# Kernel optimization log

Hardware: AMD Instinct MI355X
Metric: run time of the kernel (lower is better)

The kernel has to match this reference:

```python
import jax, jax.numpy as jnp
import numpy as np

B = 8192
SIZES = [784, 1024, 512, 10]
LR = 0.001          # update_rate default in forward
CYCLES = 60         # hardcoded in PCN.forward


def _xavier(k, shape):
    # torch.nn.init.xavier_uniform_ for 2D: fan_in=shape[1], fan_out=shape[0]
    bound = np.sqrt(6.0 / (shape[0] + shape[1])).astype(np.float32)
    return jax.random.uniform(k, shape, jnp.float32, -bound, bound)


def setup_inputs() -> dict:
    key = jax.random.key(0)
    ks = jax.random.split(key, 7)
    input_data = jax.random.uniform(ks[0], (B, SIZES[0]), jnp.float32)
    s1 = _xavier(ks[1], (B, SIZES[1]))
    s2 = _xavier(ks[2], (B, SIZES[2]))
    s3 = _xavier(ks[3], (B, SIZES[3]))
    W1 = _xavier(ks[4], (SIZES[0], SIZES[1]))
    W2 = _xavier(ks[5], (SIZES[1], SIZES[2]))
    W3 = _xavier(ks[6], (SIZES[2], SIZES[3]))
    return dict(input_data=input_data, s1=s1, s2=s2, s3=s3, W1=W1, W2=W2, W3=W3)


def _sig_prime(x):
    s = jax.nn.sigmoid(x)
    return s * (1.0 - s)


def reference(input_data, s1, s2, s3, W1, W2, W3):
    def cycle(carry, _):
        s1, s2, s3, _ = carry
        # predictions: layer i predicts layer i-1 via sigmoid(state_i) @ W_i.T
        p0 = jax.nn.sigmoid(s1) @ W1.T            # (B, 784)
        p1 = jax.nn.sigmoid(s2) @ W2.T            # (B, 1024)
        p2 = jax.nn.sigmoid(s3) @ W3.T            # (B, 512)
        e0 = input_data - p0
        e1 = s1 - p1
        e2 = s2 - p2
        # state updates (batched matmul (W.T @ e) == e @ W)
        s1n = s1 + LR * (-e1 + _sig_prime(s1) * (e0 @ W1))
        s2n = s2 + LR * (-e2 + _sig_prime(s2) * (e1 @ W2))
        s3n = s3 + LR * (_sig_prime(s3) * (e2 @ W3))  # last layer: no -e term
        return (s1n, s2n, s3n, p0), None

    p0_init = jnp.zeros((B, SIZES[0]), jnp.float32)
    (s1, s2, s3, p0_last), _ = jax.lax.scan(
        cycle, (s1, s2, s3, p0_init), None, length=CYCLES)
    # returns (last-layer state, predictions[0] from the final cycle)
    return s3, p0_last
```

## Files before the change

### kernel.cpp

```cpp
#include <hip/hip_runtime.h>
#include <hip/hip_bf16.h>

typedef __bf16 bf16x8 __attribute__((ext_vector_type(8)));
typedef ushort ushort8 __attribute__((ext_vector_type(8)));
typedef float  f32x4  __attribute__((ext_vector_type(4)));

#define LR_C 0.001f
#define VMCNT(n) asm volatile("s_waitcnt vmcnt(" #n ")" ::: "memory")
#define CFENCE() asm volatile("" ::: "memory")

__device__ __forceinline__ float sigf(float x){ return 1.0f/(1.0f + __expf(-x)); }
__device__ __forceinline__ ushort f2bu(float x){ __hip_bfloat16 h = __float2bfloat16(x); return *(ushort*)&h; }
__device__ __forceinline__ float bu2f(ushort u){ __hip_bfloat16 h = *(__hip_bfloat16*)&u; return __bfloat162float(h); }

__device__ __forceinline__ void gload_lds16(const void* g, void* l){
  __builtin_amdgcn_global_load_lds(
      (const __attribute__((address_space(1))) void*)g,
      (__attribute__((address_space(3))) void*)l, 16, 0, 0);
}


__global__ void k_cvt_bf16(__hip_bfloat16* dst, const float* src, int n){
  int i = blockIdx.x*256 + threadIdx.x;
  if (i < n) dst[i] = __float2bfloat16(src[i]);
}

__global__ void k_cvt_pad(__hip_bfloat16* dst, const float* src, int rows, int cs, int cd){
  int i = blockIdx.x*256 + threadIdx.x;
  if (i >= rows*cd) return;
  int r = i / cd, c = i % cd;
  float v = (c < cs) ? src[r*cs + c] : 0.0f;
  dst[i] = __float2bfloat16(v);
}

__global__ void k_transpose(__hip_bfloat16* dst, const float* src, int sr, int sc, int dstride){
  int i = blockIdx.x*256 + threadIdx.x;
  if (i >= sc*dstride) return;
  int n = i / dstride, j = i % dstride;
  float v = (j < sr) ? src[j*sc + n] : 0.0f;
  dst[i] = __float2bfloat16(v);
}

__global__ void k_init_state(ushort* sf, __hip_bfloat16* A, const float* s, int n){
  int i = blockIdx.x*256 + threadIdx.x;
  if (i >= n) return;
  float v = s[i];
  sf[i] = f2bu(v);
  A[i] = __float2bfloat16(sigf(v));
}

__global__ void k_init_s3(float* s3f, __hip_bfloat16* A3, const float* s3){
  int i = blockIdx.x*256 + threadIdx.x;
  if (i >= 8192*32) return;
  int b = i >> 5, c = i & 31;
  if (c < 10){
    float v = s3[b*10 + c];
    s3f[b*10 + c] = v;
    A3[i] = __float2bfloat16(sigf(v));
  } else {
    A3[i] = __float2bfloat16(0.0f);
  }
}

__global__ void k_zero_bf16(__hip_bfloat16* p, int n){
  int i = blockIdx.x*256 + threadIdx.x;
  if (i < n) p[i] = __float2bfloat16(0.0f);
}

__global__ void k_copy_f32(float* dst, const float* src, int n){
  int i = blockIdx.x*256 + threadIdx.x;
  if (i < n) dst[i] = src[i];
}


__device__ __forceinline__ void gemm128(
    const ushort* __restrict__ A, const ushort* __restrict__ B,
    int lda, int ldb, int K, int Nclamp,
    int brow, int bcol, int t, ushort* As, ushort* Bs, f32x4 (&acc)[4][4])
{
  const int w    = t >> 6;
  const int lane = t & 63;
  const int wr   = (w >> 1) * 64;
  const int wc   = (w & 1) * 64;
  const int fr   = lane & 15;
  const int ks   = (lane >> 4) * 8;
  const int rks  = ks ^ ((fr & 3) << 3);

#pragma unroll
  for (int m=0;m<4;m++)
#pragma unroll
    for (int n=0;n<4;n++){ acc[m][n][0]=0.f; acc[m][n][1]=0.f; acc[m][n][2]=0.f; acc[m][n][3]=0.f; }

  const int arow = t >> 2;
  const int acol = ((t & 3) * 8) ^ ((arow & 3) << 3);
  const ushort* gA  = A + (size_t)(brow + arow) * lda + acol;
  const ushort* gA2 = gA + (size_t)64 * lda;
  int rb  = bcol + arow;      if (rb  > Nclamp-1) rb  = Nclamp-1;
  int rb2 = bcol + 64 + arow; if (rb2 > Nclamp-1) rb2 = Nclamp-1;
  const ushort* gB  = B + (size_t)rb  * ldb + acol;
  const ushort* gB2 = B + (size_t)rb2 * ldb + acol;

  auto STAGE = [&](int buf, int k0){
    ushort* Ab = As + buf*4096;
    ushort* Bb = Bs + buf*4096;
    gload_lds16(gA  + k0, Ab + w*512);
    gload_lds16(gA2 + k0, Ab + 2048 + w*512);
    gload_lds16(gB  + k0, Bb + w*512);
    gload_lds16(gB2 + k0, Bb + 2048 + w*512);
  };

  const int nt = K >> 5;
  STAGE(0, 0);
  if (nt > 1) STAGE(1, 32);
  if (nt > 2) STAGE(2, 64);

  int cur = 0;
  for (int tk = 0; tk < nt; ++tk){
    const int rem = nt - 1 - tk;
    if (rem >= 2)      { VMCNT(8); }
    else if (rem == 1) { VMCNT(4); }
    else               { VMCNT(0); }
    __builtin_amdgcn_s_barrier();
    CFENCE();

    const ushort* Ab = As + cur*4096;
    const ushort* Bb = Bs + cur*4096;
    bf16x8 af[4], bfv[4];
#pragma unroll
    for (int m=0;m<4;m++) af[m]  = *(const bf16x8*)&Ab[(wr + m*16 + fr)*32 + rks];
#pragma unroll
    for (int n=0;n<4;n++) bfv[n] = *(const bf16x8*)&Bb[(wc + n*16 + fr)*32 + rks];
#pragma unroll
    for (int m=0;m<4;m++)
#pragma unroll
      for (int n=0;n<4;n++)
        acc[m][n] = __builtin_amdgcn_mfma_f32_16x16x32_bf16(af[m], bfv[n], acc[m][n], 0, 0, 0);

    CFENCE();
    __builtin_amdgcn_s_barrier();
    CFENCE();
    if (tk + 3 < nt) STAGE(cur, (tk+3)*32);
    cur = cur + 1; if (cur == 3) cur = 0;
  }
}

__device__ __forceinline__ void stageC(const f32x4 (&acc)[4][4], int t, ushort* Cs){
  const int w = t >> 6, lane = t & 63;
  const int wr = (w >> 1) * 64, wc = (w & 1) * 64;
  const int fr = lane & 15, r4 = (lane >> 4) * 4;
#pragma unroll
  for (int m=0;m<4;m++){
#pragma unroll
    for (int j=0;j<4;j++){
      int r = wr + m*16 + r4 + j;
      int sw = (r & 3) << 3;
#pragma unroll
      for (int n=0;n<4;n++){
        int c = wc + n*16 + fr;
        Cs[r*128 + (c ^ sw)] = f2bu(acc[m][n][j]);
      }
    }
  }
}

__device__ __forceinline__ void blockmap(int lid, int nbx, int& brow, int& bcol){
  int by = (lid & 7) + 8 * ((lid >> 3) / nbx);
  int bx = (lid >> 3) % nbx;
  brow = by * 128; bcol = bx * 128;
}


__global__ __launch_bounds__(256, 3)
void fusedD1(int base,
             const ushort* __restrict__ A1, const ushort* __restrict__ W1b,
             const ushort* __restrict__ inb, ushort* __restrict__ e0, float* p0out,
             const ushort* __restrict__ e1b, const ushort* __restrict__ W2T,
             ushort* __restrict__ s2f, const ushort* __restrict__ e2b,
             ushort* __restrict__ A2,
             const ushort* __restrict__ W3T, float* __restrict__ s3f,
             ushort* __restrict__ A3)
{
  __shared__ __align__(16) ushort lds[3*4096*2];
  ushort* As = lds;
  ushort* Bs = lds + 3*4096;
  ushort* Cs = lds;
  const int bid = blockIdx.x + base;
  const int t = threadIdx.x;
  const int lr = t >> 4, lc = (t & 15) * 8;
  f32x4 acc[4][4];

  if (bid < 448){
    int brow, bcol; blockmap(bid, 7, brow, bcol);
    gemm128(A1, W1b, 1024, 1024, 1024, 784, brow, bcol, t, As, Bs, acc);
    stageC(acc, t, Cs); __syncthreads();
#pragma unroll
    for (int it=0; it<8; ++it){
      int r = it*16 + lr, gr = brow + r, gc = bcol + lc;
      if (gc < 784){
        ushort8 ib = *(const ushort8*)&inb[(size_t)gr*784 + gc];
        ushort8 g  = *(const ushort8*)&Cs[r*128 + (lc ^ ((r&3)<<3))];
        ushort8 e; float pv0,pv1,pv2,pv3,pv4,pv5,pv6,pv7;
        pv0=bu2f(g[0]); pv1=bu2f(g[1]); pv2=bu2f(g[2]); pv3=bu2f(g[3]);
        pv4=bu2f(g[4]); pv5=bu2f(g[5]); pv6=bu2f(g[6]); pv7=bu2f(g[7]);
        e[0]=f2bu(bu2f(ib[0])-pv0); e[1]=f2bu(bu2f(ib[1])-pv1);
        e[2]=f2bu(bu2f(ib[2])-pv2); e[3]=f2bu(bu2f(ib[3])-pv3);
        e[4]=f2bu(bu2f(ib[4])-pv4); e[5]=f2bu(bu2f(ib[5])-pv5);
        e[6]=f2bu(bu2f(ib[6])-pv6); e[7]=f2bu(bu2f(ib[7])-pv7);
        *(ushort8*)&e0[(size_t)gr*800 + gc] = e;
        if (p0out){
          f32x4 lo = {pv0,pv1,pv2,pv3}, hi = {pv4,pv5,pv6,pv7};
          *(f32x4*)&p0out[(size_t)gr*784 + gc]     = lo;
          *(f32x4*)&p0out[(size_t)gr*784 + gc + 4] = hi;
        }
      }
    }
  } else if (bid < 704){
    int brow, bcol; blockmap(bid - 448, 4, brow, bcol);
    gemm128(e1b, W2T, 1024, 1024, 1024, 512, brow, bcol, t, As, Bs, acc);
    stageC(acc, t, Cs); __syncthreads();
#pragma unroll
    for (int it=0; it<8; ++it){
      int r = it*16 + lr, gr = brow + r, gc = bcol + lc;
      size_t ix = (size_t)gr*512 + gc;
      ushort8 sv = *(const ushort8*)&s2f[ix];
      ushort8 e2 = *(const ushort8*)&e2b[ix];
      ushort8 g = *(const ushort8*)&Cs[r*128 + (lc ^ ((r&3)<<3))];
      ushort8 a2o, so;
#pragma unroll
      for (int k=0;k<8;k++){
        float s = bu2f(sv[k]); float a = sigf(s);
        float ap = a*(1.0f-a);
        float d = LR_C*(-bu2f(e2[k]) + ap*bu2f(g[k]));
        so[k] = f2bu(s + d);
        a2o[k] = f2bu(a + ap*d);
      }
      *(ushort8*)&s2f[ix] = so;
      *(ushort8*)&A2[ix] = a2o;
    }
  } else {
    int brow = (bid - 704) * 128;
    gemm128(e2b, W3T, 512, 512, 512, 16, brow, 0, t, As, Bs, acc);
    const int w = t >> 6, lane = t & 63;
    const int wr = (w >> 1) * 64, wc = (w & 1) * 64;
    const int fr = lane & 15, r4 = (lane >> 4) * 4;
    const int orow0 = brow + wr + r4, ocol0 = wc + fr;
#pragma unroll
    for (int m=0;m<4;m++)
#pragma unroll
      for (int n=0;n<4;n++){
        int col = ocol0 + n*16;
        if (col >= 10) continue;
#pragma unroll
        for (int j=0;j<4;j++){
          int row = orow0 + m*16 + j;
          float s = s3f[(size_t)row*10 + col];
          float a = sigf(s);
          float ap = a*(1.0f-a);
          float d = LR_C*(ap*acc[m][n][j]);
          s3f[(size_t)row*10 + col] = s + d;
          A3[(size_t)row*32 + col] = f2bu(a + ap*d);
        }
      }
  }
}

__global__ __launch_bounds__(256, 3)
void fusedD2(const ushort* __restrict__ A2, const ushort* __restrict__ W2b,
             const ushort* __restrict__ e0, const ushort* __restrict__ W1T,
             ushort* __restrict__ s1f, ushort* __restrict__ A1,
             ushort* __restrict__ e1b,
             const ushort* __restrict__ A3, const ushort* __restrict__ W3b,
             const ushort* __restrict__ s2f, ushort* __restrict__ e2b)
{
  __shared__ __align__(16) ushort lds[3*4096*2];
  ushort* As = lds;
  ushort* Bs = lds + 3*4096;
  ushort* Cs = lds;
  const int bid = blockIdx.x;
  const int t = threadIdx.x;
  const int lr = t >> 4, lc = (t & 15) * 8;
  f32x4 acc[4][4];

  if (bid < 512){
    int brow, bcol; blockmap(bid, 8, brow, bcol);
    gemm128(A2, W2b, 512, 512, 512, 1024, brow, bcol, t, As, Bs, acc);
    stageC(acc, t, Cs); __syncthreads();
#pragma unroll
    for (int it=0; it<8; ++it){
      int r = it*16 + lr, gr = brow + r, gc = bcol + lc;
      size_t ix = (size_t)gr*1024 + gc;
      ushort8 sv = *(const ushort8*)&s1f[ix];
      ushort8 g = *(const ushort8*)&Cs[r*128 + (lc ^ ((r&3)<<3))];
      ushort8 e1o;
#pragma unroll
      for (int k=0;k<8;k++) e1o[k] = f2bu(bu2f(sv[k]) - bu2f(g[k]));
      *(ushort8*)&e1b[ix] = e1o;
    }
    __syncthreads();
    gemm128(e0, W1T, 800, 800, 800, 1024, brow, bcol, t, As, Bs, acc);
    stageC(acc, t, Cs); __syncthreads();
#pragma unroll
    for (int it=0; it<8; ++it){
      int r = it*16 + lr, gr = brow + r, gc = bcol + lc;
      size_t ix = (size_t)gr*1024 + gc;
      ushort8 e1 = *(const ushort8*)&e1b[ix];
      ushort8 sv = *(const ushort8*)&s1f[ix];
      ushort8 g = *(const ushort8*)&Cs[r*128 + (lc ^ ((r&3)<<3))];
      ushort8 a1o, so;
#pragma unroll
      for (int k=0;k<8;k++){
        float s = bu2f(sv[k]);
        float a = sigf(s);
        float ap = a*(1.0f-a);
        float d = LR_C*(-bu2f(e1[k]) + ap*bu2f(g[k]));
        so[k] = f2bu(s + d);
        a1o[k] = f2bu(a + ap*d);
      }
      *(ushort8*)&s1f[ix] = so;
      *(ushort8*)&A1[ix]  = a1o;
    }
  } else {
    int brow, bcol; blockmap(bid - 512, 4, brow, bcol);
    gemm128(A3, W3b, 32, 32, 32, 512, brow, bcol, t, As, Bs, acc);
    stageC(acc, t, Cs); __syncthreads();
#pragma unroll
    for (int it=0; it<8; ++it){
      int r = it*16 + lr, gr = brow + r, gc = bcol + lc;
      size_t ix = (size_t)gr*512 + gc;
      ushort8 sv = *(const ushort8*)&s2f[ix];
      ushort8 g = *(const ushort8*)&Cs[r*128 + (lc ^ ((r&3)<<3))];
      ushort8 e2o;
#pragma unroll
      for (int k=0;k<8;k++) e2o[k] = f2bu(bu2f(sv[k]) - bu2f(g[k]));
      *(ushort8*)&e2b[ix] = e2o;
    }
  }
}


extern "C" void kernel_launch(void* const* d_in, const int* in_sizes, int n_in,
                              void* d_out, int out_size, void* d_ws, size_t ws_size,
                              hipStream_t stream) {
  const float* input = (const float*)d_in[0];
  const float* s1    = (const float*)d_in[1];
  const float* s2    = (const float*)d_in[2];
  const float* s3    = (const float*)d_in[3];
  const float* W1    = (const float*)d_in[4];
  const float* W2    = (const float*)d_in[5];
  const float* W3    = (const float*)d_in[6];
  float* out = (float*)d_out;

  char* ws = (char*)d_ws;
  size_t off = 0;
  auto take = [&](size_t bytes)->char*{
    char* p = ws + off;
    off = (off + bytes + 255) & ~(size_t)255;
    return p;
  };

  ushort* s1f = (ushort*)take(8192ull*1024*2);
  ushort* s2f = (ushort*)take(8192ull*512*2);
  float*  s3f = (float*)take(8192ull*10*4);
  __hip_bfloat16* A1  = (__hip_bfloat16*)take(8192ull*1024*2);
  __hip_bfloat16* A2  = (__hip_bfloat16*)take(8192ull*512*2);
  __hip_bfloat16* A3  = (__hip_bfloat16*)take(8192ull*32*2);
  __hip_bfloat16* e0  = (__hip_bfloat16*)take(8192ull*800*2);
  __hip_bfloat16* e1b = (__hip_bfloat16*)take(8192ull*1024*2);
  __hip_bfloat16* e2b = (__hip_bfloat16*)take(8192ull*512*2);
  __hip_bfloat16* inb = (__hip_bfloat16*)take(8192ull*784*2);
  __hip_bfloat16* W1b = (__hip_bfloat16*)take(784ull*1024*2);
  __hip_bfloat16* W2b = (__hip_bfloat16*)take(1024ull*512*2);
  __hip_bfloat16* W3b = (__hip_bfloat16*)take(512ull*32*2);
  __hip_bfloat16* W1T = (__hip_bfloat16*)take(1024ull*800*2);
  __hip_bfloat16* W2T = (__hip_bfloat16*)take(512ull*1024*2);
  __hip_bfloat16* W3T = (__hip_bfloat16*)take(16ull*512*2);

  auto cdiv = [](int a, int b){ return (a + b - 1) / b; };

  k_cvt_bf16 <<<cdiv(8192*784,256),256,0,stream>>>(inb, input, 8192*784);
  k_cvt_bf16 <<<cdiv(784*1024,256),256,0,stream>>>(W1b, W1, 784*1024);
  k_cvt_bf16 <<<cdiv(1024*512,256),256,0,stream>>>(W2b, W2, 1024*512);
  k_cvt_pad  <<<cdiv(512*32,256),256,0,stream>>>(W3b, W3, 512, 10, 32);
  k_transpose<<<cdiv(1024*800,256),256,0,stream>>>(W1T, W1, 784, 1024, 800);
  k_transpose<<<cdiv(512*1024,256),256,0,stream>>>(W2T, W2, 1024, 512, 1024);
  k_zero_bf16<<<cdiv(16*512,256),256,0,stream>>>(W3T, 16*512);
  k_transpose<<<cdiv(10*512,256),256,0,stream>>>(W3T, W3, 512, 10, 512);
  k_init_state<<<cdiv(8192*1024,256),256,0,stream>>>(s1f, A1, s1, 8192*1024);
  k_init_state<<<cdiv(8192*512,256),256,0,stream>>>(s2f, A2, s2, 8192*512);
  k_init_s3  <<<cdiv(8192*32,256),256,0,stream>>>(s3f, A3, s3);
  k_zero_bf16<<<cdiv(8192*800,256),256,0,stream>>>(e0, 8192*800);

  for (int c = 0; c < 60; ++c){
    float* p0_dst = (c == 59) ? (out + 8192*10) : nullptr;
    if (c == 0){
      fusedD1<<<448, 256, 0, stream>>>(0, (const ushort*)A1, (const ushort*)W1b,
          (const ushort*)inb, (ushort*)e0, p0_dst,
          (const ushort*)e1b, (const ushort*)W2T, s2f, (const ushort*)e2b,
          (ushort*)A2, (const ushort*)W3T, s3f, (ushort*)A3);
    } else {
      fusedD1<<<768, 256, 0, stream>>>(0, (const ushort*)A1, (const ushort*)W1b,
          (const ushort*)inb, (ushort*)e0, p0_dst,
          (const ushort*)e1b, (const ushort*)W2T, s2f, (const ushort*)e2b,
          (ushort*)A2, (const ushort*)W3T, s3f, (ushort*)A3);
    }
    fusedD2<<<768, 256, 0, stream>>>((const ushort*)A2, (const ushort*)W2b,
        (const ushort*)e0, (const ushort*)W1T, s1f, (ushort*)A1, (ushort*)e1b,
        (const ushort*)A3, (const ushort*)W3b, (const ushort*)s2f, (ushort*)e2b);
  }
  fusedD1<<<320, 256, 0, stream>>>(448, (const ushort*)A1, (const ushort*)W1b,
      (const ushort*)inb, (ushort*)e0, nullptr,
      (const ushort*)e1b, (const ushort*)W2T, s2f, (const ushort*)e2b,
      (ushort*)A2, (const ushort*)W3T, s3f, (ushort*)A3);

  k_copy_f32<<<cdiv(8192*10,256),256,0,stream>>>(out, s3f, 8192*10);
}
```

Baseline: 4.729 ms.

## Load GEMM B operand directly from global into registers, bypassing LDS

New measurement: 7.055 ms. +49.2%, slower.

```diff
diff --git a/kernel.cpp b/kernel.cpp
--- a/kernel.cpp
+++ b/kernel.cpp
@@ -76,7 +76,7 @@
 __device__ __forceinline__ void gemm128(
     const ushort* __restrict__ A, const ushort* __restrict__ B,
     int lda, int ldb, int K, int Nclamp,
-    int brow, int bcol, int t, ushort* As, ushort* Bs, f32x4 (&acc)[4][4])
+    int brow, int bcol, int t, ushort* As, f32x4 (&acc)[4][4])
 {
   const int w    = t >> 6;
   const int lane = t & 63;
@@ -95,52 +95,65 @@
   const int acol = ((t & 3) * 8) ^ ((arow & 3) << 3);
   const ushort* gA  = A + (size_t)(brow + arow) * lda + acol;
   const ushort* gA2 = gA + (size_t)64 * lda;
-  int rb  = bcol + arow;      if (rb  > Nclamp-1) rb  = Nclamp-1;
-  int rb2 = bcol + 64 + arow; if (rb2 > Nclamp-1) rb2 = Nclamp-1;
-  const ushort* gB  = B + (size_t)rb  * ldb + acol;
-  const ushort* gB2 = B + (size_t)rb2 * ldb + acol;
-
-  auto STAGE = [&](int buf, int k0){
+
+  const ushort* gBp[4];
+#pragma unroll
+  for (int n=0;n<4;n++){
+    int rn = bcol + wc + n*16 + fr;
+    if (rn > Nclamp-1) rn = Nclamp-1;
+    gBp[n] = B + (size_t)rn * ldb + ks;
+  }
+
+  auto STAGE_A = [&](int buf, int k0){
     ushort* Ab = As + buf*4096;
-    ushort* Bb = Bs + buf*4096;
     gload_lds16(gA  + k0, Ab + w*512);
     gload_lds16(gA2 + k0, Ab + 2048 + w*512);
-    gload_lds16(gB  + k0, Bb + w*512);
-    gload_lds16(gB2 + k0, Bb + 2048 + w*512);
   };
+  auto LOADB = [&](bf16x8 (&S)[4], int tkk){
+    const size_t ko = (size_t)tkk * 32;
+#pragma unroll
+    for (int n=0;n<4;n++) S[n] = *(const bf16x8*)(gBp[n] + ko);
+  };
 
   const int nt = K >> 5;
-  STAGE(0, 0);
-  if (nt > 1) STAGE(1, 32);
-  if (nt > 2) STAGE(2, 64);
-
-  int cur = 0;
-  for (int tk = 0; tk < nt; ++tk){
+  bf16x8 b0[4], b1[4], b2[4];
+
+  STAGE_A(0, 0);
+  LOADB(b0, 0);
+  if (nt > 1){ STAGE_A(1, 32); LOADB(b1, 1); }
+  if (nt > 2){ STAGE_A(2, 64); }
+  CFENCE();
+
+  auto GSTEP = [&](int tk, bf16x8 (&BC)[4], bf16x8 (&BN)[4]){
+    if (tk >= nt) return;
     const int rem = nt - 1 - tk;
     if (rem >= 2)      { VMCNT(8); }
-    else if (rem == 1) { VMCNT(4); }
+    else if (rem == 1) { VMCNT(6); }
     else               { VMCNT(0); }
     __builtin_amdgcn_s_barrier();
     CFENCE();
-
-    const ushort* Ab = As + cur*4096;
-    const ushort* Bb = Bs + cur*4096;
-    bf16x8 af[4], bfv[4];
-#pragma unroll
-    for (int m=0;m<4;m++) af[m]  = *(const bf16x8*)&Ab[(wr + m*16 + fr)*32 + rks];
-#pragma unroll
-    for (int n=0;n<4;n++) bfv[n] = *(const bf16x8*)&Bb[(wc + n*16 + fr)*32 + rks];
+    if (tk + 2 < nt) LOADB(BN, tk + 2);
+    CFENCE();
+    const ushort* Ab = As + (tk % 3) * 4096;
+    bf16x8 af[4];
+#pragma unroll
+    for (int m=0;m<4;m++) af[m] = *(const bf16x8*)&Ab[(wr + m*16 + fr)*32 + rks];
 #pragma unroll
     for (int m=0;m<4;m++)
 #pragma unroll
       for (int n=0;n<4;n++)
-        acc[m][n] = __builtin_amdgcn_mfma_f32_16x16x32_bf16(af[m], bfv[n], acc[m][n], 0, 0, 0);
-
+        acc[m][n] = __builtin_amdgcn_mfma_f32_16x16x32_bf16(af[m], BC[n], acc[m][n], 0, 0, 0);
     CFENCE();
     __builtin_amdgcn_s_barrier();
     CFENCE();
-    if (tk + 3 < nt) STAGE(cur, (tk+3)*32);
-    cur = cur + 1; if (cur == 3) cur = 0;
+    if (tk + 3 < nt) STAGE_A(tk % 3, (tk+3)*32);
+    CFENCE();
+  };
+
+  for (int tk0 = 0; tk0 < nt; tk0 += 3){
+    GSTEP(tk0,     b0, b2);
+    GSTEP(tk0 + 1, b1, b0);
+    GSTEP(tk0 + 2, b2, b1);
   }
 }
 
@@ -180,9 +193,8 @@
              const ushort* __restrict__ W3T, float* __restrict__ s3f,
              ushort* __restrict__ A3)
 {
-  __shared__ __align__(16) ushort lds[3*4096*2];
+  __shared__ __align__(16) ushort lds[16384];
   ushort* As = lds;
-  ushort* Bs = lds + 3*4096;
   ushort* Cs = lds;
   const int bid = blockIdx.x + base;
   const int t = threadIdx.x;
@@ -191,7 +203,7 @@
 
   if (bid < 448){
     int brow, bcol; blockmap(bid, 7, brow, bcol);
-    gemm128(A1, W1b, 1024, 1024, 1024, 784, brow, bcol, t, As, Bs, acc);
+    gemm128(A1, W1b, 1024, 1024, 1024, 784, brow, bcol, t, As, acc);
     stageC(acc, t, Cs); __syncthreads();
 #pragma unroll
     for (int it=0; it<8; ++it){
@@ -216,7 +228,7 @@
     }
   } else if (bid < 704){
     int brow, bcol; blockmap(bid - 448, 4, brow, bcol);
-    gemm128(e1b, W2T, 1024, 1024, 1024, 512, brow, bcol, t, As, Bs, acc);
+    gemm128(e1b, W2T, 1024, 1024, 1024, 512, brow, bcol, t, As, acc);
     stageC(acc, t, Cs); __syncthreads();
 #pragma unroll
     for (int it=0; it<8; ++it){
@@ -239,7 +251,7 @@
     }
   } else {
     int brow = (bid - 704) * 128;
-    gemm128(e2b, W3T, 512, 512, 512, 16, brow, 0, t, As, Bs, acc);
+    gemm128(e2b, W3T, 512, 512, 512, 16, brow, 0, t, As, acc);
     const int w = t >> 6, lane = t & 63;
     const int wr = (w >> 1) * 64, wc = (w & 1) * 64;
     const int fr = lane & 15, r4 = (lane >> 4) * 4;
@@ -272,9 +284,8 @@
              const ushort* __restrict__ A3, const ushort* __restrict__ W3b,
              const ushort* __restrict__ s2f, ushort* __restrict__ e2b)
 {
-  __shared__ __align__(16) ushort lds[3*4096*2];
+  __shared__ __align__(16) ushort lds[16384];
   ushort* As = lds;
-  ushort* Bs = lds + 3*4096;
   ushort* Cs = lds;
   const int bid = blockIdx.x;
   const int t = threadIdx.x;
@@ -283,7 +294,7 @@
 
   if (bid < 512){
     int brow, bcol; blockmap(bid, 8, brow, bcol);
-    gemm128(A2, W2b, 512, 512, 512, 1024, brow, bcol, t, As, Bs, acc);
+    gemm128(A2, W2b, 512, 512, 512, 1024, brow, bcol, t, As, acc);
     stageC(acc, t, Cs); __syncthreads();
 #pragma unroll
     for (int it=0; it<8; ++it){
@@ -297,7 +308,7 @@
       *(ushort8*)&e1b[ix] = e1o;
     }
     __syncthreads();
-    gemm128(e0, W1T, 800, 800, 800, 1024, brow, bcol, t, As, Bs, acc);
+    gemm128(e0, W1T, 800, 800, 800, 1024, brow, bcol, t, As, acc);
     stageC(acc, t, Cs); __syncthreads();
 #pragma unroll
     for (int it=0; it<8; ++it){
@@ -321,7 +332,7 @@
     }
   } else {
     int brow, bcol; blockmap(bid - 512, 4, brow, bcol);
-    gemm128(A3, W3b, 32, 32, 32, 512, brow, bcol, t, As, Bs, acc);
+    gemm128(A3, W3b, 32, 32, 32, 512, brow, bcol, t, As, acc);
     stageC(acc, t, Cs); __syncthreads();
 #pragma unroll
     for (int it=0; it<8; ++it){
```
